# Kernel tuning notes

Measured on AMD Instinct MI355X. Metric: run time of the kernel, lower is better.

The kernel has to match this reference:

```python
import jax, jax.numpy as jnp
import numpy as np

N = 50000
IN_DIM = 512
HID = 64
E = 800000


def setup_inputs() -> dict:
    key = jax.random.key(0)
    k1, k2, k3, k4 = jax.random.split(key, 4)
    x = jax.random.normal(k1, (N, IN_DIM), dtype=jnp.float32)
    edge_index = jax.random.randint(k2, (2, E), 0, N, dtype=jnp.int32)
    # Glorot-ish init for linear weights
    W1 = jax.random.normal(k3, (IN_DIM, HID), dtype=jnp.float32) / np.sqrt(IN_DIM)
    b1 = jnp.zeros((HID,), dtype=jnp.float32)
    W2 = jax.random.normal(k4, (HID, HID), dtype=jnp.float32) / np.sqrt(HID)
    b2 = jnp.zeros((HID,), dtype=jnp.float32)
    return {"x": x, "edge_index": edge_index, "W1": W1, "b1": b1, "W2": W2, "b2": b2}


def gcn_conv(x, src, dst, norm, W, b, n):
    # x' = D^{-1/2} (A+I) D^{-1/2} x W + b  (PyG GCNConv with self-loops)
    h = x @ W                                  # [N, out] dense GEMM
    msg = h[src] * norm[:, None]               # gather + scale per edge
    out = jax.ops.segment_sum(msg, dst, num_segments=n)  # scatter-add
    return out + b


def reference(x, edge_index, W1, b1, W2, b2):
    n = x.shape[0]
    loop = jnp.arange(n, dtype=edge_index.dtype)
    src = jnp.concatenate([edge_index[0], loop])  # add self-loops
    dst = jnp.concatenate([edge_index[1], loop])
    deg = jax.ops.segment_sum(jnp.ones_like(src, dtype=x.dtype), dst, num_segments=n)
    dinv = jnp.where(deg > 0, jax.lax.rsqrt(deg), 0.0)
    norm = dinv[src] * dinv[dst]               # symmetric normalization per edge
    h = gcn_conv(x, src, dst, norm, W1, b1, n)
    h = jax.nn.relu(h)
    # dropout is identity in eval mode (reference baseline)
    z = gcn_conv(h, src, dst, norm, W2, b2, n)
    return z
```

## Files before the change

### kernel.cpp

```cpp
#include <hip/hip_runtime.h>
#include <stdint.h>


typedef __attribute__((ext_vector_type(8))) short short8;
typedef __attribute__((ext_vector_type(4))) float f32x4;

__device__ __forceinline__ int wave_incl_scan(int v, int lane) {
#pragma unroll
  for (int d = 1; d < 64; d <<= 1) {
    int o = __shfl_up(v, d);
    if (lane >= d) v += o;
  }
  return v;
}

__device__ __forceinline__ uint32_t bf16_rne(float f) {
  uint32_t u = __float_as_uint(f);
  return (u + 0x7FFFu + ((u >> 16) & 1u)) >> 16;
}

__global__ __launch_bounds__(256) void hist_kernel(const int* __restrict__ dst, int E,
                                                   int* __restrict__ counts) {
  int i = blockIdx.x * 256 + threadIdx.x;
  if (i < E) atomicAdd(&counts[dst[i]], 1);
}

__global__ __launch_bounds__(256) void bsum_kernel(const int* __restrict__ counts,
                                                   int* __restrict__ bsum, int n) {
  int i = blockIdx.x * 256 + threadIdx.x;
  int c = (i < n) ? ((counts[i] + 7) & ~7) : 0;
#pragma unroll
  for (int d = 32; d > 0; d >>= 1) c += __shfl_down(c, d);
  __shared__ int ws[4];
  if ((threadIdx.x & 63) == 0) ws[threadIdx.x >> 6] = c;
  __syncthreads();
  if (threadIdx.x == 0) bsum[blockIdx.x] = ws[0] + ws[1] + ws[2] + ws[3];
}

__global__ __launch_bounds__(256) void scan_bsums_kernel(const int* __restrict__ bsum,
                                                         int* __restrict__ boff, int nb) {
  int t = threadIdx.x, lane = t & 63;
  int v = (t < nb) ? bsum[t] : 0;
  int incl = wave_incl_scan(v, lane);
  __shared__ int wsum[4];
  if (lane == 63) wsum[t >> 6] = incl;
  __syncthreads();
  int pre = 0;
  for (int j = 0; j < (t >> 6); ++j) pre += wsum[j];
  if (t < nb) boff[t] = pre + incl - v;
}

__global__ __launch_bounds__(256) void scan_apply_kernel(const int* __restrict__ counts,
                                                         const int* __restrict__ boff,
                                                         int* __restrict__ offsets,
                                                         int* __restrict__ cursor,
                                                         float* __restrict__ dinv,
                                                         int2* __restrict__ meta, int n) {
  int b = blockIdx.x, t = threadIdx.x, lane = t & 63;
  int i = b * 256 + t;
  int craw = (i < n) ? counts[i] : 0;
  int c = (craw + 7) & ~7;
  int incl = wave_incl_scan(c, lane);
  __shared__ int wsum[4];
  if (lane == 63) wsum[t >> 6] = incl;
  __syncthreads();
  int pre = 0;
  for (int j = 0; j < (t >> 6); ++j) pre += wsum[j];
  int excl = boff[b] + pre + incl - c;
  if (i < n) {
    offsets[i] = excl;
    cursor[i] = excl;
    dinv[i] = rsqrtf((float)(craw + 1));
    for (int k = craw; k < c; ++k) meta[excl + k] = make_int2(0, 0);
    if (i == n - 1) offsets[n] = excl + c;
  }
}

__global__ __launch_bounds__(256) void fill_kernel(const int* __restrict__ src,
                                                   const int* __restrict__ dst, int E,
                                                   int* __restrict__ cursor,
                                                   const float* __restrict__ dinv,
                                                   int2* __restrict__ meta) {
  int i = blockIdx.x * 256 + threadIdx.x;
  if (i < E) {
    int s = src[i];
    int d = dst[i];
    int pos = atomicAdd(&cursor[d], 1);
    float w = dinv[s] * dinv[d];
    meta[pos] = make_int2(s, __float_as_int(w));
  }
}

__global__ __launch_bounds__(256) void wfrag_kernel(const float* __restrict__ W1,
                                                    const float* __restrict__ W2,
                                                    short8* __restrict__ wh1,
                                                    short8* __restrict__ wl1,
                                                    short8* __restrict__ wh2,
                                                    short8* __restrict__ wl2,
                                                    int K1, int K2) {
  int idx = blockIdx.x * 256 + threadIdx.x;
  int tot1 = (K1 >> 5) * 256;
  int tot2 = (K2 >> 5) * 256;
  const float* W;
  short8 *wh, *wl;
  if (idx < tot1) {
    W = W1; wh = wh1; wl = wl1;
  } else if (idx < tot1 + tot2) {
    idx -= tot1;
    W = W2; wh = wh2; wl = wl2;
  } else {
    return;
  }
  int lane = idx & 63;
  int ct = (idx >> 6) & 3;
  int kt = idx >> 8;
  int m = lane & 15, q = lane >> 4;
  int col = ct * 16 + m;
  short8 h, l;
#pragma unroll
  for (int j = 0; j < 8; ++j) {
    float f = W[(size_t)(kt * 32 + q * 8 + j) * 64 + col];
    uint32_t hb = bf16_rne(f);
    float hf = __uint_as_float(hb << 16);
    float lo = f - hf;
    h[j] = (short)hb;
    l[j] = (short)bf16_rne(lo);
  }
  wh[idx] = h;
  wl[idx] = l;
}

__global__ __launch_bounds__(256) void gemm_mfma_kernel(const float* __restrict__ A,
                                                        const short8* __restrict__ wh,
                                                        const short8* __restrict__ wl,
                                                        ushort* __restrict__ outb,
                                                        int n, int K) {
  const int t = threadIdx.x;
  const int w = t >> 6, lane = t & 63;
  const int m = lane & 15, q = lane >> 4;
  const int row0 = blockIdx.x * 128 + w * 32;
  int r0 = row0 + m;
  int r1 = row0 + 16 + m;
  if (r0 >= n) r0 = n - 1;
  if (r1 >= n) r1 = n - 1;
  const float* ap0 = A + (size_t)r0 * K + q * 8;
  const float* ap1 = A + (size_t)r1 * K + q * 8;
  const short8* whp = wh + lane;
  const short8* wlp = wl + lane;
  const int nkt = K >> 5;
  f32x4 acc[2][4];
#pragma unroll
  for (int g = 0; g < 2; ++g)
#pragma unroll
    for (int c = 0; c < 4; ++c) acc[g][c] = 0.f;

  float4 xa0 = *(const float4*)(ap0);
  float4 xa1 = *(const float4*)(ap0 + 4);
  float4 xb0 = *(const float4*)(ap1);
  float4 xb1 = *(const float4*)(ap1 + 4);
  short8 bh[4] = {whp[0], whp[64], whp[128], whp[192]};
  short8 bl[4] = {wlp[0], wlp[64], wlp[128], wlp[192]};

  auto cvt = [&](const float4& u0, const float4& u1, short8& hi, short8& lo) {
    float xf[8] = {u0.x, u0.y, u0.z, u0.w, u1.x, u1.y, u1.z, u1.w};
#pragma unroll
    for (int j = 0; j < 8; ++j) {
      uint32_t hb = bf16_rne(xf[j]);
      float hf = __uint_as_float(hb << 16);
      hi[j] = (short)hb;
      lo[j] = (short)bf16_rne(xf[j] - hf);
    }
  };
  auto compute = [&]() {
    short8 ah0, al0, ah1, al1;
    cvt(xa0, xa1, ah0, al0);
    cvt(xb0, xb1, ah1, al1);
#pragma unroll
    for (int c = 0; c < 4; ++c) {
      acc[0][c] = __builtin_amdgcn_mfma_f32_16x16x32_bf16(ah0, bh[c], acc[0][c], 0, 0, 0);
      acc[1][c] = __builtin_amdgcn_mfma_f32_16x16x32_bf16(ah1, bh[c], acc[1][c], 0, 0, 0);
    }
#pragma unroll
    for (int c = 0; c < 4; ++c) {
      acc[0][c] = __builtin_amdgcn_mfma_f32_16x16x32_bf16(ah0, bl[c], acc[0][c], 0, 0, 0);
      acc[1][c] = __builtin_amdgcn_mfma_f32_16x16x32_bf16(ah1, bl[c], acc[1][c], 0, 0, 0);
    }
#pragma unroll
    for (int c = 0; c < 4; ++c) {
      acc[0][c] = __builtin_amdgcn_mfma_f32_16x16x32_bf16(al0, bh[c], acc[0][c], 0, 0, 0);
      acc[1][c] = __builtin_amdgcn_mfma_f32_16x16x32_bf16(al1, bh[c], acc[1][c], 0, 0, 0);
    }
  };

  for (int kt = 0; kt < nkt - 1; ++kt) {
    const float* an0 = ap0 + 32;
    const float* an1 = ap1 + 32;
    float4 nxa0 = *(const float4*)(an0);
    float4 nxa1 = *(const float4*)(an0 + 4);
    float4 nxb0 = *(const float4*)(an1);
    float4 nxb1 = *(const float4*)(an1 + 4);
    const short8* whn = whp + 256;
    const short8* wln = wlp + 256;
    short8 nh[4] = {whn[0], whn[64], whn[128], whn[192]};
    short8 nl[4] = {wln[0], wln[64], wln[128], wln[192]};
    compute();
    xa0 = nxa0; xa1 = nxa1; xb0 = nxb0; xb1 = nxb1;
#pragma unroll
    for (int c = 0; c < 4; ++c) { bh[c] = nh[c]; bl[c] = nl[c]; }
    ap0 = an0; ap1 = an1; whp = whn; wlp = wln;
  }
  compute();

#pragma unroll
  for (int g = 0; g < 2; ++g)
#pragma unroll
    for (int i = 0; i < 4; ++i) {
      int rr = row0 + g * 16 + q * 4 + i;
      if (rr < n) {
        ushort* op = outb + (size_t)rr * 64 + m;
        op[0]  = (ushort)bf16_rne(acc[g][0][i]);
        op[16] = (ushort)bf16_rne(acc[g][1][i]);
        op[32] = (ushort)bf16_rne(acc[g][2][i]);
        op[48] = (ushort)bf16_rne(acc[g][3][i]);
      }
    }
}

__global__ __launch_bounds__(256) void agg_kernel(const ushort* __restrict__ H,
                                                  const int* __restrict__ offsets,
                                                  const int2* __restrict__ meta,
                                                  const float* __restrict__ dinv,
                                                  const float* __restrict__ bias,
                                                  float* __restrict__ out, int n, int do_relu) {
  const int t = threadIdx.x;
  const int sl = t & 7;
  const int v = blockIdx.x * 32 + (t >> 3);
  if (v >= n) return;
  const float dv = dinv[v];
  const float dvv = dv * dv;
  float acc[8];
  {
    uint4 hv = *(const uint4*)&H[(size_t)v * 64 + (sl << 3)];
    uint32_t u[4] = {hv.x, hv.y, hv.z, hv.w};
#pragma unroll
    for (int j = 0; j < 4; ++j) {
      acc[2 * j]     = __uint_as_float(u[j] << 16) * dvv;
      acc[2 * j + 1] = __uint_as_float(u[j] & 0xFFFF0000u) * dvv;
    }
  }
  const int e0 = offsets[v], e1 = offsets[v + 1];
  const int4* p = (const int4*)(meta + e0);
  int rem = (e1 - e0) >> 3;
  int4 a0, a1, a2, a3;
  if (rem > 0) { a0 = p[0]; a1 = p[1]; a2 = p[2]; a3 = p[3]; }
  auto gather8 = [&](int4 c0, int4 c1, int4 c2, int4 c3) {
    int s[8] = {c0.x, c0.z, c1.x, c1.z, c2.x, c2.z, c3.x, c3.z};
    int wi[8] = {c0.y, c0.w, c1.y, c1.w, c2.y, c2.w, c3.y, c3.w};
    uint4 raw[8];
#pragma unroll
    for (int j = 0; j < 8; ++j) raw[j] = *(const uint4*)&H[(size_t)s[j] * 64 + (sl << 3)];
#pragma unroll
    for (int j = 0; j < 8; ++j) {
      const float wgt = __int_as_float(wi[j]);
      uint32_t u[4] = {raw[j].x, raw[j].y, raw[j].z, raw[j].w};
#pragma unroll
      for (int k = 0; k < 4; ++k) {
        acc[2 * k]     = fmaf(__uint_as_float(u[k] << 16), wgt, acc[2 * k]);
        acc[2 * k + 1] = fmaf(__uint_as_float(u[k] & 0xFFFF0000u), wgt, acc[2 * k + 1]);
      }
    }
  };
  while (rem > 1) {
    int4 b0 = p[4], b1 = p[5], b2 = p[6], b3 = p[7];
    gather8(a0, a1, a2, a3);
    a0 = b0; a1 = b1; a2 = b2; a3 = b3;
    p += 4;
    --rem;
  }
  if (rem == 1) gather8(a0, a1, a2, a3);
  const float4 blo = *(const float4*)&bias[sl << 3];
  const float4 bhi = *(const float4*)&bias[(sl << 3) + 4];
  float bb[8] = {blo.x, blo.y, blo.z, blo.w, bhi.x, bhi.y, bhi.z, bhi.w};
#pragma unroll
  for (int j = 0; j < 8; ++j) {
    acc[j] += bb[j];
    if (do_relu) acc[j] = fmaxf(acc[j], 0.f);
  }
  float* op = out + (size_t)v * 64 + (sl << 3);
  *(float4*)op = make_float4(acc[0], acc[1], acc[2], acc[3]);
  *(float4*)(op + 4) = make_float4(acc[4], acc[5], acc[6], acc[7]);
}

extern "C" void kernel_launch(void* const* d_in, const int* in_sizes, int n_in,
                              void* d_out, int out_size, void* d_ws, size_t ws_size,
                              hipStream_t stream) {
  const float* x = (const float*)d_in[0];
  const int* ei = (const int*)d_in[1];
  const float* W1 = (const float*)d_in[2];
  const float* b1 = (const float*)d_in[3];
  const float* W2 = (const float*)d_in[4];
  const float* b2 = (const float*)d_in[5];
  float* out = (float*)d_out;

  const int HID = in_sizes[3];
  const int IN_DIM = in_sizes[2] / HID;
  const int N = in_sizes[0] / IN_DIM;
  const int E = in_sizes[1] / 2;
  const int NB = (N + 255) / 256;
  const size_t META_MAX = (size_t)E + 8 * (size_t)N;

  uint8_t* p = (uint8_t*)d_ws;
  auto alloc = [&](size_t bytes) {
    void* r = (void*)p;
    p += (bytes + 255) & ~(size_t)255;
    return r;
  };
  int* counts = (int*)alloc((size_t)N * 4);
  int* offsets = (int*)alloc((size_t)(N + 1) * 4);
  int* cursor = (int*)alloc((size_t)N * 4);
  int* bsum = (int*)alloc((size_t)NB * 4);
  int* boff = (int*)alloc((size_t)NB * 4);
  float* dinv = (float*)alloc((size_t)N * 4);
  int2* meta = (int2*)alloc(META_MAX * 8);
  ushort* hb = (ushort*)alloc((size_t)N * HID * 2);
  float* h = (float*)alloc((size_t)N * HID * 4);
  short8* wh1 = (short8*)alloc((size_t)(IN_DIM >> 5) * 256 * 16);
  short8* wl1 = (short8*)alloc((size_t)(IN_DIM >> 5) * 256 * 16);
  short8* wh2 = (short8*)alloc((size_t)(HID >> 5) * 256 * 16);
  short8* wl2 = (short8*)alloc((size_t)(HID >> 5) * 256 * 16);

  const int* srcp = ei;
  const int* dstp = ei + E;

  hipMemsetAsync(counts, 0, (size_t)N * 4, stream);
  hist_kernel<<<(E + 255) / 256, 256, 0, stream>>>(dstp, E, counts);
  bsum_kernel<<<NB, 256, 0, stream>>>(counts, bsum, N);
  scan_bsums_kernel<<<1, 256, 0, stream>>>(bsum, boff, NB);
  scan_apply_kernel<<<NB, 256, 0, stream>>>(counts, boff, offsets, cursor, dinv, meta, N);
  fill_kernel<<<(E + 255) / 256, 256, 0, stream>>>(srcp, dstp, E, cursor, dinv, meta);

  const int wtot = (IN_DIM >> 5) * 256 + (HID >> 5) * 256;
  wfrag_kernel<<<(wtot + 255) / 256, 256, 0, stream>>>(W1, W2, wh1, wl1, wh2, wl2,
                                                       IN_DIM, HID);

  gemm_mfma_kernel<<<(N + 127) / 128, 256, 0, stream>>>(x, wh1, wl1, hb, N, IN_DIM);
  agg_kernel<<<(N + 31) / 32, 256, 0, stream>>>(hb, offsets, meta, dinv, b1, h, N, 1);
  gemm_mfma_kernel<<<(N + 127) / 128, 256, 0, stream>>>(h, wh2, wl2, hb, N, HID);
  agg_kernel<<<(N + 31) / 32, 256, 0, stream>>>(hb, offsets, meta, dinv, b2, out, N, 0);
}
```

Measured before the change: 301.2 us.

## Stage GEMM tiles through LDS with async loads and double-buffer aggregation gathers

The GEMM now copies the A tiles (XOR-swizzled) and the split-bf16 weight fragments into double-buffered shared memory using global_load_lds async copies. Each block covers 64 rows instead of 128, with 16 rows per wave, which doubles the grid and halves the accumulators per wave. The aggregation kernel now issues the next batch of 8 neighbour gathers before consuming the current batch, so more memory loads are in flight. The cost is more registers in the aggregation and a __syncthreads plus LDS traffic on every k-step of the GEMM.

```diff
diff --git a/kernel.cpp b/kernel.cpp
--- a/kernel.cpp
+++ b/kernel.cpp
@@ -4,6 +4,12 @@
 
 typedef __attribute__((ext_vector_type(8))) short short8;
 typedef __attribute__((ext_vector_type(4))) float f32x4;
+
+__device__ __forceinline__ void async16(void* lds, const void* g) {
+  __builtin_amdgcn_global_load_lds(
+      (const __attribute__((address_space(1))) uint32_t*)g,
+      (__attribute__((address_space(3))) uint32_t*)lds, 16, 0, 0);
+}
 
 __device__ __forceinline__ int wave_incl_scan(int v, int lane) {
 #pragma unroll
@@ -135,95 +141,91 @@
                                                         const short8* __restrict__ wl,
                                                         ushort* __restrict__ outb,
                                                         int n, int K) {
+  __shared__ float4 xs[2][512];
+  __shared__ short8 bsm[2][512];
   const int t = threadIdx.x;
   const int w = t >> 6, lane = t & 63;
   const int m = lane & 15, q = lane >> 4;
-  const int row0 = blockIdx.x * 128 + w * 32;
-  int r0 = row0 + m;
-  int r1 = row0 + 16 + m;
-  if (r0 >= n) r0 = n - 1;
-  if (r1 >= n) r1 = n - 1;
-  const float* ap0 = A + (size_t)r0 * K + q * 8;
-  const float* ap1 = A + (size_t)r1 * K + q * 8;
-  const short8* whp = wh + lane;
-  const short8* wlp = wl + lane;
+  const int row0 = blockIdx.x * 64;
   const int nkt = K >> 5;
-  f32x4 acc[2][4];
-#pragma unroll
-  for (int g = 0; g < 2; ++g)
-#pragma unroll
-    for (int c = 0; c < 4; ++c) acc[g][c] = 0.f;
-
-  float4 xa0 = *(const float4*)(ap0);
-  float4 xa1 = *(const float4*)(ap0 + 4);
-  float4 xb0 = *(const float4*)(ap1);
-  float4 xb1 = *(const float4*)(ap1 + 4);
-  short8 bh[4] = {whp[0], whp[64], whp[128], whp[192]};
-  short8 bl[4] = {wlp[0], wlp[64], wlp[128], wlp[192]};
-
-  auto cvt = [&](const float4& u0, const float4& u1, short8& hi, short8& lo) {
-    float xf[8] = {u0.x, u0.y, u0.z, u0.w, u1.x, u1.y, u1.z, u1.w};
-#pragma unroll
-    for (int j = 0; j < 8; ++j) {
-      uint32_t hb = bf16_rne(xf[j]);
-      float hf = __uint_as_float(hb << 16);
-      hi[j] = (short)hb;
-      lo[j] = (short)bf16_rne(xf[j] - hf);
+
+  const float* sga[2];
+#pragma unroll
+  for (int i = 0; i < 2; ++i) {
+    int L = w * 128 + i * 64 + lane;
+    int row = L >> 3, ps = L & 7;
+    int kc = ps ^ (row & 7);
+    int gr = row0 + row;
+    if (gr >= n) gr = n - 1;
+    sga[i] = A + (size_t)gr * K + (kc << 2);
+  }
+
+  auto stage = [&](int kt, int buf) {
+#pragma unroll
+    for (int i = 0; i < 2; ++i)
+      async16(&xs[buf][w * 128 + i * 64], sga[i] + kt * 32);
+#pragma unroll
+    for (int i = 0; i < 2; ++i) {
+      int M0 = w * 128 + i * 64;
+      const short8* src = (M0 < 256) ? (wh + (size_t)kt * 256 + M0 + lane)
+                                     : (wl + (size_t)kt * 256 + (M0 - 256) + lane);
+      async16(&bsm[buf][M0], src);
     }
   };
-  auto compute = [&]() {
-    short8 ah0, al0, ah1, al1;
-    cvt(xa0, xa1, ah0, al0);
-    cvt(xb0, xb1, ah1, al1);
+
+  f32x4 acc[4];
+#pragma unroll
+  for (int c = 0; c < 4; ++c) acc[c] = 0.f;
+
+  stage(0, 0);
+  const int row = w * 16 + m;
+  const int sl0 = row * 8 + ((2 * q) ^ (row & 7));
+  const int sl1 = row * 8 + ((2 * q + 1) ^ (row & 7));
+  for (int kt = 0; kt < nkt; ++kt) {
+    const int cur = kt & 1;
+    __syncthreads();
+    if (kt + 1 < nkt) stage(kt + 1, cur ^ 1);
+    float4 u0 = xs[cur][sl0];
+    float4 u1 = xs[cur][sl1];
+    short8 ah, al;
+    {
+      float xf[8] = {u0.x, u0.y, u0.z, u0.w, u1.x, u1.y, u1.z, u1.w};
+#pragma unroll
+      for (int j = 0; j < 8; ++j) {
+        uint32_t hb = bf16_rne(xf[j]);
+        float hf = __uint_as_float(hb << 16);
+        ah[j] = (short)hb;
+        al[j] = (short)bf16_rne(xf[j] - hf);
+      }
+    }
+    short8 bh[4], bl[4];
 #pragma unroll
     for (int c = 0; c < 4; ++c) {
-      acc[0][c] = __builtin_amdgcn_mfma_f32_16x16x32_bf16(ah0, bh[c], acc[0][c], 0, 0, 0);
-      acc[1][c] = __builtin_amdgcn_mfma_f32_16x16x32_bf16(ah1, bh[c], acc[1][c], 0, 0, 0);
-    }
-#pragma unroll
-    for (int c = 0; c < 4; ++c) {
-      acc[0][c] = __builtin_amdgcn_mfma_f32_16x16x32_bf16(ah0, bl[c], acc[0][c], 0, 0, 0);
-      acc[1][c] = __builtin_amdgcn_mfma_f32_16x16x32_bf16(ah1, bl[c], acc[1][c], 0, 0, 0);
-    }
-#pragma unroll
-    for (int c = 0; c < 4; ++c) {
-      acc[0][c] = __builtin_amdgcn_mfma_f32_16x16x32_bf16(al0, bh[c], acc[0][c], 0, 0, 0);
-      acc[1][c] = __builtin_amdgcn_mfma_f32_16x16x32_bf16(al1, bh[c], acc[1][c], 0, 0, 0);
-    }
-  };
-
-  for (int kt = 0; kt < nkt - 1; ++kt) {
-    const float* an0 = ap0 + 32;
-    const float* an1 = ap1 + 32;
-    float4 nxa0 = *(const float4*)(an0);
-    float4 nxa1 = *(const float4*)(an0 + 4);
-    float4 nxb0 = *(const float4*)(an1);
-    float4 nxb1 = *(const float4*)(an1 + 4);
-    const short8* whn = whp + 256;
-    const short8* wln = wlp + 256;
-    short8 nh[4] = {whn[0], whn[64], whn[128], whn[192]};
-    short8 nl[4] = {wln[0], wln[64], wln[128], wln[192]};
-    compute();
-    xa0 = nxa0; xa1 = nxa1; xb0 = nxb0; xb1 = nxb1;
-#pragma unroll
-    for (int c = 0; c < 4; ++c) { bh[c] = nh[c]; bl[c] = nl[c]; }
-    ap0 = an0; ap1 = an1; whp = whn; wlp = wln;
-  }
-  compute();
-
-#pragma unroll
-  for (int g = 0; g < 2; ++g)
-#pragma unroll
-    for (int i = 0; i < 4; ++i) {
-      int rr = row0 + g * 16 + q * 4 + i;
-      if (rr < n) {
-        ushort* op = outb + (size_t)rr * 64 + m;
-        op[0]  = (ushort)bf16_rne(acc[g][0][i]);
-        op[16] = (ushort)bf16_rne(acc[g][1][i]);
-        op[32] = (ushort)bf16_rne(acc[g][2][i]);
-        op[48] = (ushort)bf16_rne(acc[g][3][i]);
-      }
-    }
+      bh[c] = bsm[cur][c * 64 + lane];
+      bl[c] = bsm[cur][256 + c * 64 + lane];
+    }
+#pragma unroll
+    for (int c = 0; c < 4; ++c)
+      acc[c] = __builtin_amdgcn_mfma_f32_16x16x32_bf16(ah, bh[c], acc[c], 0, 0, 0);
+#pragma unroll
+    for (int c = 0; c < 4; ++c)
+      acc[c] = __builtin_amdgcn_mfma_f32_16x16x32_bf16(ah, bl[c], acc[c], 0, 0, 0);
+#pragma unroll
+    for (int c = 0; c < 4; ++c)
+      acc[c] = __builtin_amdgcn_mfma_f32_16x16x32_bf16(al, bh[c], acc[c], 0, 0, 0);
+  }
+
+#pragma unroll
+  for (int i = 0; i < 4; ++i) {
+    int rr = row0 + w * 16 + q * 4 + i;
+    if (rr < n) {
+      ushort* op = outb + (size_t)rr * 64 + m;
+      op[0]  = (ushort)bf16_rne(acc[0][i]);
+      op[16] = (ushort)bf16_rne(acc[1][i]);
+      op[32] = (ushort)bf16_rne(acc[2][i]);
+      op[48] = (ushort)bf16_rne(acc[3][i]);
+    }
+  }
 }
 
 __global__ __launch_bounds__(256) void agg_kernel(const ushort* __restrict__ H,
@@ -251,18 +253,20 @@
   const int e0 = offsets[v], e1 = offsets[v + 1];
   const int4* p = (const int4*)(meta + e0);
   int rem = (e1 - e0) >> 3;
-  int4 a0, a1, a2, a3;
-  if (rem > 0) { a0 = p[0]; a1 = p[1]; a2 = p[2]; a3 = p[3]; }
-  auto gather8 = [&](int4 c0, int4 c1, int4 c2, int4 c3) {
-    int s[8] = {c0.x, c0.z, c1.x, c1.z, c2.x, c2.z, c3.x, c3.z};
-    int wi[8] = {c0.y, c0.w, c1.y, c1.w, c2.y, c2.w, c3.y, c3.w};
-    uint4 raw[8];
-#pragma unroll
-    for (int j = 0; j < 8; ++j) raw[j] = *(const uint4*)&H[(size_t)s[j] * 64 + (sl << 3)];
+
+  int4 ma[4], mb[4];
+  uint4 ra[8], rb[8];
+  auto gath = [&](const int4* c, uint4* r) {
+    int s[8] = {c[0].x, c[0].z, c[1].x, c[1].z, c[2].x, c[2].z, c[3].x, c[3].z};
+#pragma unroll
+    for (int j = 0; j < 8; ++j) r[j] = *(const uint4*)&H[(size_t)s[j] * 64 + (sl << 3)];
+  };
+  auto consume = [&](const int4* c, const uint4* r) {
+    int wi[8] = {c[0].y, c[0].w, c[1].y, c[1].w, c[2].y, c[2].w, c[3].y, c[3].w};
 #pragma unroll
     for (int j = 0; j < 8; ++j) {
       const float wgt = __int_as_float(wi[j]);
-      uint32_t u[4] = {raw[j].x, raw[j].y, raw[j].z, raw[j].w};
+      uint32_t u[4] = {r[j].x, r[j].y, r[j].z, r[j].w};
 #pragma unroll
       for (int k = 0; k < 4; ++k) {
         acc[2 * k]     = fmaf(__uint_as_float(u[k] << 16), wgt, acc[2 * k]);
@@ -270,14 +274,26 @@
       }
     }
   };
+
+  if (rem > 0) {
+#pragma unroll
+    for (int j = 0; j < 4; ++j) ma[j] = p[j];
+    gath(ma, ra);
+  }
   while (rem > 1) {
-    int4 b0 = p[4], b1 = p[5], b2 = p[6], b3 = p[7];
-    gather8(a0, a1, a2, a3);
-    a0 = b0; a1 = b1; a2 = b2; a3 = b3;
+#pragma unroll
+    for (int j = 0; j < 4; ++j) mb[j] = p[4 + j];
+    gath(mb, rb);
+    consume(ma, ra);
+#pragma unroll
+    for (int j = 0; j < 4; ++j) ma[j] = mb[j];
+#pragma unroll
+    for (int j = 0; j < 8; ++j) ra[j] = rb[j];
     p += 4;
     --rem;
   }
-  if (rem == 1) gather8(a0, a1, a2, a3);
+  if (rem == 1) consume(ma, ra);
+
   const float4 blo = *(const float4*)&bias[sl << 3];
   const float4 bhi = *(const float4*)&bias[(sl << 3) + 4];
   float bb[8] = {blo.x, blo.y, blo.z, blo.w, bhi.x, bhi.y, bhi.z, bhi.w};
@@ -343,8 +359,8 @@
   wfrag_kernel<<<(wtot + 255) / 256, 256, 0, stream>>>(W1, W2, wh1, wl1, wh2, wl2,
                                                        IN_DIM, HID);
 
-  gemm_mfma_kernel<<<(N + 127) / 128, 256, 0, stream>>>(x, wh1, wl1, hb, N, IN_DIM);
+  gemm_mfma_kernel<<<(N + 63) / 64, 256, 0, stream>>>(x, wh1, wl1, hb, N, IN_DIM);
   agg_kernel<<<(N + 31) / 32, 256, 0, stream>>>(hb, offsets, meta, dinv, b1, h, N, 1);
-  gemm_mfma_kernel<<<(N + 127) / 128, 256, 0, stream>>>(h, wh2, wl2, hb, N, HID);
+  gemm_mfma_kernel<<<(N + 63) / 64, 256, 0, stream>>>(h, wh2, wl2, hb, N, HID);
   agg_kernel<<<(N + 31) / 32, 256, 0, stream>>>(hb, offsets, meta, dinv, b2, out, N, 0);
 }
```

Result: no change. 306.7 us (+1.8%).
